# Performance work log

Measured on AMD Instinct MI355X. Metric: run time of the kernel, lower is better.

Reference implementation:

```python
import jax, jax.numpy as jnp
import numpy as np

KSIZE = 3          # self.ksize
SCALE = 10.0       # self.softmax_scale
EPS = 1e-4         # escape_NaN, added per-element before the reduce_sum
MASK_DS = 8        # int_fs[3] != 32 -> mask downsampled by 8*rate


def extract_patches(x, k, s):
    """torch extract_image_patches with 'same' padding.
    x: [B,C,H,W] -> [B, L, C, k, k] with L = out_h*out_w (row-major positions),
    matching unfold -> view(B,C,k,k,L) -> permute(0,4,1,2,3)."""
    B, C, H, W = x.shape
    oh, ow = -(-H // s), -(-W // s)
    pr = max(0, (oh - 1) * s + k - H)
    pc = max(0, (ow - 1) * s + k - W)
    pt, pl = pr // 2, pc // 2
    xp = jnp.pad(x, ((0, 0), (0, 0), (pt, pr - pt), (pl, pc - pl)))
    sl = [xp[:, :, i:i + (oh - 1) * s + 1:s, j:j + (ow - 1) * s + 1:s]
          for i in range(k) for j in range(k)]          # k*k static slices
    p = jnp.stack(sl, axis=2).reshape(B, C, k, k, oh, ow)
    return p.transpose(0, 4, 5, 1, 2, 3).reshape(B, oh * ow, C, k, k)


def contextual_attention_score(f, b, mask):
    # rate=1 -> both F.interpolate(scale_factor=1.0) calls are identity.
    B, C, Hf, Wf = f.shape
    Hb, Wb = b.shape[2], b.shape[3]
    # background patches used as correlation filters: [B, Lb, C, 3, 3]
    w = extract_patches(b, KSIZE, 1)
    # mask: nearest downsample by 8 == strided subsampling
    mask_s = mask[:, :, ::MASK_DS, ::MASK_DS]
    m = extract_patches(mask_s, KSIZE, 1)[0]            # [Lb, 1, 3, 3] (batch 0 only, as in source)
    pm = jnp.mean(jax.lax.stop_gradient(m), axis=(1, 2, 3))
    mm = (pm == 0.0).astype(f.dtype).reshape(1, -1, 1, 1)  # [1, Lb, 1, 1]
    # L2-normalize each filter (EPS added per element before the sum, as in source)
    denom = jnp.sqrt(jnp.sum(w * w + EPS, axis=(2, 3, 4), keepdims=True))
    wn = w / denom
    # per-sample conv2d(xi_padded, wi_normed) == patch cross-correlation:
    fp = extract_patches(f, KSIZE, 1)                   # [B, Lf, C, 3, 3]
    y = jnp.einsum('bqckl,bpckl->bpq', fp, wn)          # [B, Lb, Lf]
    y = y.reshape(B, Hb * Wb, Hf, Wf) * mm
    y = jax.nn.softmax(y * SCALE, axis=1) * mm
    return y                                            # module returns `score`


def setup_inputs():
    key = jax.random.key(0)
    k1, k2 = jax.random.split(key)
    f = jax.random.normal(k1, (4, 128, 64, 64), dtype=jnp.float32)
    b = jax.random.normal(k2, (4, 128, 64, 64), dtype=jnp.float32)
    # binary inpainting mask at image resolution (1 = hole / unavailable)
    mask = jnp.zeros((4, 1, 512, 512), dtype=jnp.float32)
    mask = mask.at[:, :, 192:320, 192:320].set(1.0)
    return {"f": f, "b": b, "mask": mask}


def reference(f, b, mask):
    return contextual_attention_score(f, b, mask)
```

## Files before the change

### kernel.cpp

```cpp
#include <hip/hip_runtime.h>
#include <hip/hip_bf16.h>
#include <math.h>


typedef float f32x4 __attribute__((ext_vector_type(4)));
typedef short bf16x8 __attribute__((ext_vector_type(8)));

#define NB 4
#define NC 128
#define NP 4096ull
#define LOG2E_SCALE 14.426950408889634f
#define EPS_TERM (1152.0f * 1e-4f)

#define SZ_S      (4ull * NP * NP * 4ull)
#define SZ_BT     (4ull * NP * NC * 2ull)
#define OFF_S     1024ull
#define OFF_BT_HI (OFF_S + SZ_S + 1024ull)
#define OFF_BT_LO (OFF_BT_HI + SZ_BT)
#define OFF_FT_HI (OFF_BT_LO + SZ_BT)
#define OFF_FT_LO (OFF_FT_HI + SZ_BT)
#define OFF_NORM2 (OFF_FT_LO + SZ_BT)
#define OFF_COEF  (OFF_NORM2 + 4ull * NP * 4ull)
#define OFF_MM    (OFF_COEF + 4ull * NP * 4ull)
#define OFF_PART  (OFF_MM + NP * 4ull)
#define OFF_LINV  (OFF_PART + 4ull * 128ull * NP * 4ull)

__global__ __launch_bounds__(256) void k_norm2(const float* __restrict__ bin,
                                               float* __restrict__ norm2) {
    int idx = blockIdx.x * 256 + threadIdx.x;
    int b = idx >> 12, u = idx & 4095;
    const float* src = bin + (size_t)b * NC * NP + u;
    float s = 0.f;
#pragma unroll 8
    for (int c = 0; c < NC; ++c) { float x = src[(size_t)c * NP]; s += x * x; }
    norm2[idx] = s;
}

__global__ __launch_bounds__(256) void k_coef(const float* __restrict__ norm2,
                                              const float* __restrict__ mask,
                                              float* __restrict__ coef,
                                              float* __restrict__ mmArr) {
    int idx = blockIdx.x * 256 + threadIdx.x;
    int b = idx >> 12, p = idx & 4095;
    int ph = p >> 6, pw = p & 63;
    float ns = 0.f, ms = 0.f;
#pragma unroll
    for (int dy = -1; dy <= 1; ++dy)
#pragma unroll
        for (int dx = -1; dx <= 1; ++dx) {
            int hh = ph + dy, ww = pw + dx;
            if ((unsigned)hh < 64u && (unsigned)ww < 64u) {
                ns += norm2[b * 4096 + hh * 64 + ww];
                ms += mask[(size_t)(hh * 512 + ww) * 8];
            }
        }
    float mmv = (ms == 0.f) ? 1.f : 0.f;
    coef[idx] = mmv * LOG2E_SCALE / sqrtf(ns + EPS_TERM);
    if (b == 0) mmArr[p] = mmv;
}

__global__ __launch_bounds__(256) void k_convert(const float* __restrict__ fin,
                                                 const float* __restrict__ bin,
                                                 __bf16* __restrict__ bt_hi, __bf16* __restrict__ bt_lo,
                                                 __bf16* __restrict__ ft_hi, __bf16* __restrict__ ft_lo) {
    __shared__ float tile[64][65];
    int u0 = blockIdx.x * 64;
    int k0 = blockIdx.y * 64;
    int z = blockIdx.z;
    int arr = z & 1, b = z >> 1;
    const float* src = (arr ? fin : bin) + (size_t)b * NC * NP;
    __bf16* dhi = (arr ? ft_hi : bt_hi) + (size_t)b * NP * NC;
    __bf16* dlo = (arr ? ft_lo : bt_lo) + (size_t)b * NP * NC;
    int t = threadIdx.x;
#pragma unroll
    for (int i = 0; i < 16; ++i) {
        int lin = i * 256 + t;
        int kl = lin >> 6, ul = lin & 63;
        tile[kl][ul] = src[(size_t)(k0 + kl) * NP + u0 + ul];
    }
    __syncthreads();
#pragma unroll
    for (int i = 0; i < 16; ++i) {
        int lin = i * 256 + t;
        int ul = lin >> 6, kl = lin & 63;
        float x = tile[kl][ul];
        __bf16 h = (__bf16)x;
        float hf = (float)h;
        __bf16 l = (__bf16)(x - hf);
        size_t o = (size_t)(u0 + ul) * NC + (k0 + kl);
        dhi[o] = h; dlo[o] = l;
    }
}

__global__ __launch_bounds__(256) void k_matmul(const __bf16* __restrict__ bt_hi,
                                                const __bf16* __restrict__ bt_lo,
                                                const __bf16* __restrict__ ft_hi,
                                                const __bf16* __restrict__ ft_lo,
                                                float* __restrict__ S) {
    int t = threadIdx.x;
    int lane = t & 63;
    int w = t >> 6;
    int b = blockIdx.z;
    int m_base = blockIdx.y * 128 + (w >> 1) * 64;
    int n_base = blockIdx.x * 128 + (w & 1) * 64;
    int l15 = lane & 15;
    int quad = lane >> 4;
    size_t bo = (size_t)b * NP * NC;
    const __bf16* Ah = bt_hi + bo;
    const __bf16* Al = bt_lo + bo;
    const __bf16* Bh = ft_hi + bo;
    const __bf16* Bl = ft_lo + bo;

    f32x4 acc[4][4];
#pragma unroll
    for (int i = 0; i < 4; ++i)
#pragma unroll
        for (int j = 0; j < 4; ++j) acc[i][j] = (f32x4){0.f, 0.f, 0.f, 0.f};

#pragma unroll
    for (int ks = 0; ks < 4; ++ks) {
        int k = ks * 32 + quad * 8;
        bf16x8 ah[4], al[4], bh[4], bl[4];
#pragma unroll
        for (int mt = 0; mt < 4; ++mt) {
            size_t o = (size_t)(m_base + mt * 16 + l15) * NC + k;
            ah[mt] = *(const bf16x8*)(Ah + o);
            al[mt] = *(const bf16x8*)(Al + o);
        }
#pragma unroll
        for (int nt = 0; nt < 4; ++nt) {
            size_t o = (size_t)(n_base + nt * 16 + l15) * NC + k;
            bh[nt] = *(const bf16x8*)(Bh + o);
            bl[nt] = *(const bf16x8*)(Bl + o);
        }
#pragma unroll
        for (int mt = 0; mt < 4; ++mt)
#pragma unroll
            for (int nt = 0; nt < 4; ++nt) {
                acc[mt][nt] = __builtin_amdgcn_mfma_f32_16x16x32_bf16(ah[mt], bh[nt], acc[mt][nt], 0, 0, 0);
                acc[mt][nt] = __builtin_amdgcn_mfma_f32_16x16x32_bf16(ah[mt], bl[nt], acc[mt][nt], 0, 0, 0);
                acc[mt][nt] = __builtin_amdgcn_mfma_f32_16x16x32_bf16(al[mt], bh[nt], acc[mt][nt], 0, 0, 0);
            }
    }
    float* Sb = S + (size_t)b * NP * NP;
#pragma unroll
    for (int mt = 0; mt < 4; ++mt)
#pragma unroll
        for (int nt = 0; nt < 4; ++nt) {
            int col = n_base + nt * 16 + l15;
            int row0 = m_base + mt * 16 + quad * 4;
#pragma unroll
            for (int r = 0; r < 4; ++r)
                Sb[(size_t)(row0 + r) * NP + col] = acc[mt][nt][r];
        }
}

__device__ __forceinline__ f32x4 stencil9(const float* __restrict__ rowbase,
                                          int ph, int pw, int qh, int qw0) {
    f32x4 y = {0.f, 0.f, 0.f, 0.f};
#pragma unroll
    for (int dy = -1; dy <= 1; ++dy) {
        bool okh = ((unsigned)(ph + dy) < 64u) & ((unsigned)(qh + dy) < 64u);
#pragma unroll
        for (int dx = -1; dx <= 1; ++dx) {
            bool ok = okh & ((unsigned)(pw + dx) < 64u);
            const int s = dy * 64 + dx;
            ptrdiff_t off = ok ? (ptrdiff_t)s * 4097 : 0;
            f32x4 t = *(const f32x4*)(rowbase + off);
            if (!ok) t = (f32x4){0.f, 0.f, 0.f, 0.f};
            if (dx == -1 && qw0 == 0)  t.x = 0.f;
            if (dx == 1  && qw0 == 60) t.w = 0.f;
            y += t;
        }
    }
    return y;
}

__global__ __launch_bounds__(256) void k_sumexp(const float* __restrict__ S,
                                                const float* __restrict__ coef,
                                                float* __restrict__ part) {
    int t = threadIdx.x;
    int b = blockIdx.z;
    int pc = blockIdx.y;
    int q0 = blockIdx.x * 1024 + t * 4;
    int qh = q0 >> 6, qw0 = q0 & 63;
    const float* Sb = S + (size_t)b * NP * NP;
    const float* cf = coef + (b << 12);
    f32x4 acc = {0.f, 0.f, 0.f, 0.f};
    for (int pi = 0; pi < 32; ++pi) {
        int p = pc * 32 + pi;
        int ph = p >> 6, pw = p & 63;
        const float* rowbase = Sb + (size_t)p * NP + q0;
        f32x4 y = stencil9(rowbase, ph, pw, qh, qw0);
        float c = cf[p];
        acc.x += exp2f(c * y.x);
        acc.y += exp2f(c * y.y);
        acc.z += exp2f(c * y.z);
        acc.w += exp2f(c * y.w);
    }
    *(f32x4*)(part + ((size_t)(b * 128 + pc) << 12) + q0) = acc;
}

__global__ __launch_bounds__(256) void k_rsum(const float* __restrict__ part,
                                              float* __restrict__ linv) {
    int idx = blockIdx.x * 256 + threadIdx.x;
    int b = idx >> 12, q = idx & 4095;
    float s = 0.f;
    for (int pc = 0; pc < 128; ++pc) s += part[((size_t)(b * 128 + pc) << 12) + q];
    linv[idx] = 1.0f / s;
}

__global__ __launch_bounds__(256) void k_write(const float* __restrict__ S,
                                               const float* __restrict__ coef,
                                               const float* __restrict__ mmArr,
                                               const float* __restrict__ linv,
                                               float* __restrict__ out) {
    int t = threadIdx.x;
    int b = blockIdx.z;
    int pc = blockIdx.y;
    int q0 = blockIdx.x * 1024 + t * 4;
    int qh = q0 >> 6, qw0 = q0 & 63;
    const float* Sb = S + (size_t)b * NP * NP;
    float* outb = out + (size_t)b * NP * NP;
    const float* cf = coef + (b << 12);
    f32x4 L = *(const f32x4*)(linv + (b << 12) + q0);
    for (int pi = 0; pi < 32; ++pi) {
        int p = pc * 32 + pi;
        int ph = p >> 6, pw = p & 63;
        const float* rowbase = Sb + (size_t)p * NP + q0;
        f32x4 y = stencil9(rowbase, ph, pw, qh, qw0);
        float c = cf[p];
        float mv = mmArr[p];
        f32x4 o;
        o.x = exp2f(c * y.x) * mv * L.x;
        o.y = exp2f(c * y.y) * mv * L.y;
        o.z = exp2f(c * y.z) * mv * L.z;
        o.w = exp2f(c * y.w) * mv * L.w;
        *(f32x4*)(outb + (size_t)p * NP + q0) = o;
    }
}

extern "C" void kernel_launch(void* const* d_in, const int* in_sizes, int n_in,
                              void* d_out, int out_size, void* d_ws, size_t ws_size,
                              hipStream_t stream) {
    (void)in_sizes; (void)n_in; (void)out_size; (void)ws_size;
    const float* f_in = (const float*)d_in[0];
    const float* b_in = (const float*)d_in[1];
    const float* mask = (const float*)d_in[2];
    float* out = (float*)d_out;
    char* ws = (char*)d_ws;

    float*  S     = (float*)(ws + OFF_S);
    __bf16* bt_hi = (__bf16*)(ws + OFF_BT_HI);
    __bf16* bt_lo = (__bf16*)(ws + OFF_BT_LO);
    __bf16* ft_hi = (__bf16*)(ws + OFF_FT_HI);
    __bf16* ft_lo = (__bf16*)(ws + OFF_FT_LO);
    float*  norm2 = (float*)(ws + OFF_NORM2);
    float*  coef  = (float*)(ws + OFF_COEF);
    float*  mmArr = (float*)(ws + OFF_MM);
    float*  part  = (float*)(ws + OFF_PART);
    float*  linv  = (float*)(ws + OFF_LINV);

    k_norm2  <<<64, 256, 0, stream>>>(b_in, norm2);
    k_coef   <<<64, 256, 0, stream>>>(norm2, mask, coef, mmArr);
    k_convert<<<dim3(64, 2, 8), 256, 0, stream>>>(f_in, b_in, bt_hi, bt_lo, ft_hi, ft_lo);
    k_matmul <<<dim3(32, 32, 4), 256, 0, stream>>>(bt_hi, bt_lo, ft_hi, ft_lo, S);
    k_sumexp <<<dim3(4, 128, 4), 256, 0, stream>>>(S, coef, part);
    k_rsum   <<<64, 256, 0, stream>>>(part, linv);
    k_write  <<<dim3(4, 128, 4), 256, 0, stream>>>(S, coef, mmArr, linv, out);
}
```

Measured before the change: 760.6 us.

## Store scores in diagonal layout and fuse stencil, exp and sum into one pass

```diff
diff --git a/kernel.cpp b/kernel.cpp
--- a/kernel.cpp
+++ b/kernel.cpp
@@ -11,6 +11,7 @@
 #define NP 4096ull
 #define LOG2E_SCALE 14.426950408889634f
 #define EPS_TERM (1152.0f * 1e-4f)
+#define TCH 256
 
 #define SZ_S      (4ull * NP * NP * 4ull)
 #define SZ_BT     (4ull * NP * NC * 2ull)
@@ -22,8 +23,8 @@
 #define OFF_NORM2 (OFF_FT_LO + SZ_BT)
 #define OFF_COEF  (OFF_NORM2 + 4ull * NP * 4ull)
 #define OFF_MM    (OFF_COEF + 4ull * NP * 4ull)
-#define OFF_PART  (OFF_MM + NP * 4ull)
-#define OFF_LINV  (OFF_PART + 4ull * 128ull * NP * 4ull)
+#define OFF_GSUM  (OFF_MM + NP * 4ull)
+#define OFF_LINV  (OFF_GSUM + 4ull * NP * 4ull)
 
 __global__ __launch_bounds__(256) void k_norm2(const float* __restrict__ bin,
                                                float* __restrict__ norm2) {
@@ -39,7 +40,8 @@
 __global__ __launch_bounds__(256) void k_coef(const float* __restrict__ norm2,
                                               const float* __restrict__ mask,
                                               float* __restrict__ coef,
-                                              float* __restrict__ mmArr) {
+                                              float* __restrict__ mmArr,
+                                              float* __restrict__ gsum) {
     int idx = blockIdx.x * 256 + threadIdx.x;
     int b = idx >> 12, p = idx & 4095;
     int ph = p >> 6, pw = p & 63;
@@ -57,6 +59,7 @@
     float mmv = (ms == 0.f) ? 1.f : 0.f;
     coef[idx] = mmv * LOG2E_SCALE / sqrtf(ns + EPS_TERM);
     if (b == 0) mmArr[p] = mmv;
+    gsum[idx] = 0.f;
 }
 
 __global__ __launch_bounds__(256) void k_convert(const float* __restrict__ fin,
@@ -150,93 +153,88 @@
             int col = n_base + nt * 16 + l15;
             int row0 = m_base + mt * 16 + quad * 4;
 #pragma unroll
-            for (int r = 0; r < 4; ++r)
-                Sb[(size_t)(row0 + r) * NP + col] = acc[mt][nt][r];
-        }
-}
-
-__device__ __forceinline__ f32x4 stencil9(const float* __restrict__ rowbase,
-                                          int ph, int pw, int qh, int qw0) {
-    f32x4 y = {0.f, 0.f, 0.f, 0.f};
-#pragma unroll
-    for (int dy = -1; dy <= 1; ++dy) {
-        bool okh = ((unsigned)(ph + dy) < 64u) & ((unsigned)(qh + dy) < 64u);
-#pragma unroll
-        for (int dx = -1; dx <= 1; ++dx) {
-            bool ok = okh & ((unsigned)(pw + dx) < 64u);
-            const int s = dy * 64 + dx;
-            ptrdiff_t off = ok ? (ptrdiff_t)s * 4097 : 0;
-            f32x4 t = *(const f32x4*)(rowbase + off);
-            if (!ok) t = (f32x4){0.f, 0.f, 0.f, 0.f};
-            if (dx == -1 && qw0 == 0)  t.x = 0.f;
-            if (dx == 1  && qw0 == 60) t.w = 0.f;
-            y += t;
-        }
-    }
-    return y;
-}
-
-__global__ __launch_bounds__(256) void k_sumexp(const float* __restrict__ S,
-                                                const float* __restrict__ coef,
-                                                float* __restrict__ part) {
-    int t = threadIdx.x;
-    int b = blockIdx.z;
-    int pc = blockIdx.y;
-    int q0 = blockIdx.x * 1024 + t * 4;
-    int qh = q0 >> 6, qw0 = q0 & 63;
-    const float* Sb = S + (size_t)b * NP * NP;
-    const float* cf = coef + (b << 12);
-    f32x4 acc = {0.f, 0.f, 0.f, 0.f};
-    for (int pi = 0; pi < 32; ++pi) {
-        int p = pc * 32 + pi;
-        int ph = p >> 6, pw = p & 63;
-        const float* rowbase = Sb + (size_t)p * NP + q0;
-        f32x4 y = stencil9(rowbase, ph, pw, qh, qw0);
-        float c = cf[p];
-        acc.x += exp2f(c * y.x);
-        acc.y += exp2f(c * y.y);
-        acc.z += exp2f(c * y.z);
-        acc.w += exp2f(c * y.w);
-    }
-    *(f32x4*)(part + ((size_t)(b * 128 + pc) << 12) + q0) = acc;
-}
-
-__global__ __launch_bounds__(256) void k_rsum(const float* __restrict__ part,
+            for (int r = 0; r < 4; ++r) {
+                int row = row0 + r;
+                Sb[(size_t)row * NP + ((row - col) & 4095)] = acc[mt][nt][r];
+            }
+        }
+}
+
+__global__ __launch_bounds__(256) void k_pass(const float* __restrict__ SD,
+                                              const float* __restrict__ coef,
+                                              const float* __restrict__ mmArr,
+                                              float* __restrict__ out,
+                                              float* __restrict__ gsum) {
+    int orig = blockIdx.x;
+    int wg = (orig & 7) * 128 + (orig >> 3);
+    int tc = wg & 15;
+    int dc = (wg >> 4) & 15;
+    int b  = wg >> 8;
+    int t0 = tc * TCH;
+    int d  = dc * 256 + threadIdx.x;
+    int lane = threadIdx.x & 63;
+    int w = threadIdx.x >> 6;
+    const float* SDb = SD + (size_t)b * NP * NP;
+    const float* cf  = coef + (b << 12);
+    float* outb = out + (size_t)b * NP * NP;
+
+    __shared__ float win[4][TCH + 64];
+    for (int s = lane; s < TCH + 64; s += 64) win[w][s] = 0.f;
+
+#define DLOAD(i) (SDb[(size_t)((i) < 0 ? 0 : ((i) > 4095 ? 4095 : (i))) * NP + d])
+    float am1 = DLOAD(t0 - 65), a0 = DLOAD(t0 - 64), ap1 = DLOAD(t0 - 63);
+    float bm1 = DLOAD(t0 - 1),  b0 = DLOAD(t0),      bp1 = DLOAD(t0 + 1);
+    float cm1 = DLOAD(t0 + 63), c0 = DLOAD(t0 + 64), cp1 = DLOAD(t0 + 65);
+
+#pragma unroll 4
+    for (int ti = 0; ti < TCH; ++ti) {
+        int t = t0 + ti;
+        float ap2 = DLOAD(t - 62);
+        float bp2 = DLOAD(t + 2);
+        float cp2 = DLOAD(t + 66);
+        int q  = (t - d) & 4095;
+        int qw = q & 63, qh = q >> 6;
+        int pw = t & 63, ph = t >> 6;
+        bool lv = (pw > 0)  & (qw > 0);
+        bool rv = (pw < 63) & (qw < 63);
+        bool uv = (ph > 0)  & (qh > 0);
+        bool dv = (ph < 63) & (qh < 63);
+        float Vm = a0 + (lv ? am1 : 0.f) + (rv ? ap1 : 0.f);
+        float V0 = b0 + (lv ? bm1 : 0.f) + (rv ? bp1 : 0.f);
+        float Vp = c0 + (lv ? cm1 : 0.f) + (rv ? cp1 : 0.f);
+        float T  = V0 + (uv ? Vm : 0.f) + (dv ? Vp : 0.f);
+        float e  = exp2f(cf[t] * T);
+        atomicAdd(&win[w][ti + 63 - lane], e);
+        outb[(size_t)t * NP + q] = e * mmArr[t];
+        am1 = a0; a0 = ap1; ap1 = ap2;
+        bm1 = b0; b0 = bp1; bp1 = bp2;
+        cm1 = c0; c0 = cp1; cp1 = cp2;
+    }
+#undef DLOAD
+    float* gs = gsum + (b << 12);
+    int dw = dc * 256 + w * 64;
+    int qb = t0 - dw - 63;
+    for (int s = lane; s < TCH + 63; s += 64)
+        atomicAdd(&gs[(qb + s) & 4095], win[w][s]);
+}
+
+__global__ __launch_bounds__(256) void k_linv(const float* __restrict__ gsum,
                                               float* __restrict__ linv) {
     int idx = blockIdx.x * 256 + threadIdx.x;
-    int b = idx >> 12, q = idx & 4095;
-    float s = 0.f;
-    for (int pc = 0; pc < 128; ++pc) s += part[((size_t)(b * 128 + pc) << 12) + q];
-    linv[idx] = 1.0f / s;
-}
-
-__global__ __launch_bounds__(256) void k_write(const float* __restrict__ S,
-                                               const float* __restrict__ coef,
-                                               const float* __restrict__ mmArr,
-                                               const float* __restrict__ linv,
-                                               float* __restrict__ out) {
-    int t = threadIdx.x;
-    int b = blockIdx.z;
-    int pc = blockIdx.y;
-    int q0 = blockIdx.x * 1024 + t * 4;
-    int qh = q0 >> 6, qw0 = q0 & 63;
-    const float* Sb = S + (size_t)b * NP * NP;
-    float* outb = out + (size_t)b * NP * NP;
-    const float* cf = coef + (b << 12);
-    f32x4 L = *(const f32x4*)(linv + (b << 12) + q0);
-    for (int pi = 0; pi < 32; ++pi) {
-        int p = pc * 32 + pi;
-        int ph = p >> 6, pw = p & 63;
-        const float* rowbase = Sb + (size_t)p * NP + q0;
-        f32x4 y = stencil9(rowbase, ph, pw, qh, qw0);
-        float c = cf[p];
-        float mv = mmArr[p];
-        f32x4 o;
-        o.x = exp2f(c * y.x) * mv * L.x;
-        o.y = exp2f(c * y.y) * mv * L.y;
-        o.z = exp2f(c * y.z) * mv * L.z;
-        o.w = exp2f(c * y.w) * mv * L.w;
-        *(f32x4*)(outb + (size_t)p * NP + q0) = o;
+    linv[idx] = 1.0f / gsum[idx];
+}
+
+__global__ __launch_bounds__(256) void k_scale(float* __restrict__ out,
+                                               const float* __restrict__ linv) {
+    const size_t NV = 4ull * NP * NP / 4ull;
+    for (size_t v = (size_t)blockIdx.x * 256 + threadIdx.x; v < NV; v += 2048ull * 256ull) {
+        size_t e0 = v << 2;
+        int q = (int)(e0 & 4095);
+        int b = (int)(e0 >> 24);
+        f32x4 x = *(f32x4*)(out + e0);
+        f32x4 L = *(const f32x4*)(linv + ((size_t)b << 12) + q);
+        x.x *= L.x; x.y *= L.y; x.z *= L.z; x.w *= L.w;
+        *(f32x4*)(out + e0) = x;
     }
 }
 
@@ -258,14 +256,14 @@
     float*  norm2 = (float*)(ws + OFF_NORM2);
     float*  coef  = (float*)(ws + OFF_COEF);
     float*  mmArr = (float*)(ws + OFF_MM);
-    float*  part  = (float*)(ws + OFF_PART);
+    float*  gsum  = (float*)(ws + OFF_GSUM);
     float*  linv  = (float*)(ws + OFF_LINV);
 
     k_norm2  <<<64, 256, 0, stream>>>(b_in, norm2);
-    k_coef   <<<64, 256, 0, stream>>>(norm2, mask, coef, mmArr);
+    k_coef   <<<64, 256, 0, stream>>>(norm2, mask, coef, mmArr, gsum);
     k_convert<<<dim3(64, 2, 8), 256, 0, stream>>>(f_in, b_in, bt_hi, bt_lo, ft_hi, ft_lo);
     k_matmul <<<dim3(32, 32, 4), 256, 0, stream>>>(bt_hi, bt_lo, ft_hi, ft_lo, S);
-    k_sumexp <<<dim3(4, 128, 4), 256, 0, stream>>>(S, coef, part);
-    k_rsum   <<<64, 256, 0, stream>>>(part, linv);
-    k_write  <<<dim3(4, 128, 4), 256, 0, stream>>>(S, coef, mmArr, linv, out);
-}
+    k_pass   <<<1024, 256, 0, stream>>>(S, coef, mmArr, out, gsum);
+    k_linv   <<<64, 256, 0, stream>>>(gsum, linv);
+    k_scale  <<<2048, 256, 0, stream>>>(out, linv);
+}
```

Measured after the change: 846.1 us. 11.2% more time.
